# Kernel optimization log

Measured on AMD Instinct MI355X. Metric: run time of the kernel, lower is better.

Reference implementation:

```python
import jax, jax.numpy as jnp
import numpy as np

DIM = 512
NUM_HEADS = 8
HEAD_DIM = DIM // NUM_HEADS
SEGMENT_LENGTHS = (1024, 2048, 4096)
DILATED_RATIOS = (1, 2, 4)
SCALE = HEAD_DIM ** -0.5
NEG_FILL = -100000000.0  # matches torch masked_fill value


def setup_inputs() -> dict:
    key = jax.random.key(0)
    ks = jax.random.split(key, 8)
    b, L = 2, 8192
    def nrm(k, shape, s=1.0):
        return jax.random.normal(k, shape, dtype=jnp.float32) * s
    return {
        "query": nrm(ks[0], (b, L, DIM)),
        "key_": nrm(ks[1], (b, L, DIM)),
        "value": nrm(ks[2], (b, L, DIM)),
        "Wq": nrm(ks[3], (DIM, DIM), DIM ** -0.5),
        "Wk": nrm(ks[4], (DIM, DIM), DIM ** -0.5),
        "Wv": nrm(ks[5], (DIM, DIM), DIM ** -0.5),
        "Wo": nrm(ks[6], (DIM, DIM), DIM ** -0.5),
        "bo": nrm(ks[7], (DIM,), 0.01),
    }


def _branch(q, k, v, sl, dr):
    """One (segment_length, dilation) branch.
    q,k,v: (b, L, H, D). Returns dense out (b, L, H, D) and lse (b, L, H),
    with uncovered positions set to (0, NEG_FILL).
    gathering/dense_to_sparse reduces, per head hd, to selecting positions
    l*dr + (hd // (H//dr)) within each segment (diagonal of the r1 x r2 block).
    """
    b, L, H, D = q.shape
    n = L // sl          # segments per sequence
    hsub = H // dr       # heads per dilation offset
    lsub = sl // dr      # kept tokens per segment
    # (lsub, H): dilated position of each kept token for each head
    pos = jnp.arange(lsub)[:, None] * dr + (jnp.arange(H) // hsub)[None, :]
    hid = jnp.arange(H)[None, :]

    def gather(x):
        xs = x.reshape(b, n, sl, H, D)
        g = xs[:, :, pos, hid, :]                  # (b, n, lsub, H, D)
        return jnp.transpose(g, (0, 1, 3, 2, 4))    # (b, n, H, lsub, D)

    qi = gather(q) * SCALE
    ki = gather(k)
    vi = gather(v)
    scores = jnp.einsum('bnhld,bnhmd->bnhlm', qi, ki)
    lse = jax.nn.logsumexp(scores, axis=-1)                                  # (b, n, H, lsub)
    p = jax.nn.softmax(scores.astype(jnp.float32), axis=-1).astype(scores.dtype)
    o = jnp.einsum('bnhlm,bnhmd->bnhld', p, vi)                              # (b, n, H, lsub, D)
    # sparse_to_dense: scatter back onto dilated positions (diag_embed)
    o_ = jnp.transpose(o, (0, 1, 3, 2, 4))                                    # (b, n, lsub, H, D)
    od = jnp.zeros((b, n, sl, H, D), o.dtype).at[:, :, pos, hid, :].set(o_)
    ld = jnp.zeros((b, n, sl, H), lse.dtype).at[:, :, pos, hid].set(
        jnp.transpose(lse, (0, 1, 3, 2)))
    ld = jnp.where(ld == 0, NEG_FILL, ld)  # masked_fill_(lse == 0, -1e8)
    return od.reshape(b, L, H, D), ld.reshape(b, L, H)


def reference(query, key_, value, Wq, Wk, Wv, Wo, bo):
    b, L, _ = query.shape
    def heads(x, W):
        return (x @ W.T).reshape(b, L, NUM_HEADS, HEAD_DIM)
    q = heads(query, Wq)
    k = heads(key_, Wk)
    v = heads(value, Wv)
    outs, lses = [], []
    for sl, dr in zip(SEGMENT_LENGTHS, DILATED_RATIOS):
        o, l = _branch(q, k, v, sl, dr)
        outs.append(o)
        lses.append(l)
    # merge branches via logsumexp-weighted combination (weights detached in torch)
    lse_stack = jnp.stack(lses, 0)            # (nb, b, L, H)
    m = lse_stack.max(0)
    w = jnp.exp(lse_stack - m)
    w = w / w.sum(0)
    w = jax.lax.stop_gradient(w)
    out = sum(o * wi[..., None] for o, wi in zip(outs, list(w)))
    out = out.reshape(b, L, DIM)
    return out @ Wo.T + bo
```

## Files before the change

### kernel.cpp

```cpp
#include <hip/hip_runtime.h>
#include <hip/hip_bf16.h>

typedef unsigned short u16;
typedef unsigned int u32;
typedef __attribute__((ext_vector_type(8))) short short8;
typedef __attribute__((ext_vector_type(4))) float floatx4;
typedef __attribute__((ext_vector_type(2))) unsigned int uint2v;

__device__ __forceinline__ float b2f(u16 u) {
    u32 x = ((u32)u) << 16;
    return __builtin_bit_cast(float, x);
}
__device__ __forceinline__ u16 f2b(float f) {
    u32 x = __builtin_bit_cast(u32, f);
    return (u16)((x + 0x7fffu + ((x >> 16) & 1u)) >> 16);
}
__device__ __forceinline__ u32 pack2(float lo, float hi) {
    float2 f; f.x = lo; f.y = hi;
    __hip_bfloat162 h = __float22bfloat162_rn(f);
    u32 r;
    __builtin_memcpy(&r, &h, 4);
    return r;
}
__device__ __forceinline__ float fexp2(float x) {
#if __has_builtin(__builtin_amdgcn_exp2f)
    return __builtin_amdgcn_exp2f(x);
#else
    return __expf(x * 0.6931471805599453f);
#endif
}

__device__ __forceinline__ uint2v pl32(u32 a, u32 b) {
    return __builtin_amdgcn_permlane32_swap(a, b, false, false);
}

__device__ __forceinline__ void gl16(const u16* g, u16* l) {
    __builtin_amdgcn_global_load_lds(
        (const __attribute__((address_space(1))) void*)g,
        (__attribute__((address_space(3))) void*)l, 16, 0, 0);
}

template<bool AF32>
__global__ __launch_bounds__(256) void gemm_bt_bias(
    const void* __restrict__ Ap, const float* __restrict__ B,
    u16* __restrict__ Cb, float* __restrict__ Cf, const float* __restrict__ bias,
    int M, int N, int K, float scale)
{
    __shared__ __align__(16) u16 a_lds[128][72];
    __shared__ __align__(16) u16 b_lds[128][72];
    const int tid = threadIdx.x;
    const int lane = tid & 63, wv = tid >> 6;
    const int quad = lane >> 4, l15 = lane & 15;
    const int tm = blockIdx.x, tn = blockIdx.y;
    const int wm = (wv >> 1) * 64, wn = (wv & 1) * 64;
    (void)M;

    floatx4 acc[4][4];
#pragma unroll
    for (int i = 0; i < 4; ++i)
#pragma unroll
        for (int j = 0; j < 4; ++j) acc[i][j] = (floatx4)0.f;

    for (int k0 = 0; k0 < K; k0 += 64) {
#pragma unroll
        for (int r = 0; r < 4; ++r) {
            int idx = r * 256 + tid;
            int row = idx >> 3, ch = (idx & 7) * 8;
            if constexpr (AF32) {
                const float* A = (const float*)Ap;
                const float* src = A + (size_t)(tm * 128 + row) * K + k0 + ch;
                float4 f0 = *(const float4*)src;
                float4 f1 = *(const float4*)(src + 4);
                uint4 pk;
                pk.x = pack2(f0.x, f0.y);
                pk.y = pack2(f0.z, f0.w);
                pk.z = pack2(f1.x, f1.y);
                pk.w = pack2(f1.z, f1.w);
                *(uint4*)&a_lds[row][ch] = pk;
            } else {
                const u16* A = (const u16*)Ap;
                *(uint4*)&a_lds[row][ch] =
                    *(const uint4*)(A + (size_t)(tm * 128 + row) * K + k0 + ch);
            }
            {
                const float* src = B + (size_t)(tn * 128 + row) * K + k0 + ch;
                float4 f0 = *(const float4*)src;
                float4 f1 = *(const float4*)(src + 4);
                uint4 pk;
                pk.x = pack2(f0.x, f0.y);
                pk.y = pack2(f0.z, f0.w);
                pk.z = pack2(f1.x, f1.y);
                pk.w = pack2(f1.z, f1.w);
                *(uint4*)&b_lds[row][ch] = pk;
            }
        }
        __syncthreads();
#pragma unroll
        for (int dc = 0; dc < 2; ++dc) {
            short8 af[4], bf[4];
#pragma unroll
            for (int mi = 0; mi < 4; ++mi)
                af[mi] = *(const short8*)&a_lds[wm + mi * 16 + l15][dc * 32 + quad * 8];
#pragma unroll
            for (int ni = 0; ni < 4; ++ni)
                bf[ni] = *(const short8*)&b_lds[wn + ni * 16 + l15][dc * 32 + quad * 8];
#pragma unroll
            for (int mi = 0; mi < 4; ++mi)
#pragma unroll
                for (int ni = 0; ni < 4; ++ni)
                    acc[mi][ni] = __builtin_amdgcn_mfma_f32_16x16x32_bf16(
                        af[mi], bf[ni], acc[mi][ni], 0, 0, 0);
        }
        __syncthreads();
    }
#pragma unroll
    for (int mi = 0; mi < 4; ++mi)
#pragma unroll
        for (int ni = 0; ni < 4; ++ni) {
            int col = tn * 128 + wn + ni * 16 + l15;
            float bb = bias ? bias[col] : 0.f;
#pragma unroll
            for (int r = 0; r < 4; ++r) {
                int row = tm * 128 + wm + mi * 16 + quad * 4 + r;
                float val = acc[mi][ni][r] * scale + bb;
                if (Cf) Cf[(size_t)row * N + col] = val;
                else    Cb[(size_t)row * N + col] = f2b(val);
            }
        }
}

__device__ __forceinline__ void decode_inst(int inst, int& b, int& s, int& h,
                                            int& sl, int& dr, int& phase)
{
    if (inst < 128)      { int j = inst;       b = j >> 6; s = (j >> 3) & 7; h = j & 7; sl = 1024; dr = 1; phase = 0;      }
    else if (inst < 192) { int j = inst - 128; b = j >> 5; s = (j >> 3) & 3; h = j & 7; sl = 2048; dr = 2; phase = h >> 2; }
    else                 { int j = inst - 192; b = j >> 4; s = (j >> 3) & 1; h = j & 7; sl = 4096; dr = 4; phase = h >> 1; }
}

__global__ __launch_bounds__(256) void gather_kv(
    const u16* __restrict__ kk, const u16* __restrict__ vv,
    u16* __restrict__ KG, u16* __restrict__ VT)
{
    int inst = blockIdx.x;
    int b, s, h, sl, dr, phase;
    decode_inst(inst, b, s, h, sl, dr, phase);
    int n0 = blockIdx.y * 32;
    __shared__ __align__(16) u16 tile[32][72];
    int tid = threadIdx.x;
    int row = tid >> 3, ch = (tid & 7) * 8;
    int n = n0 + row;
    size_t pos = (size_t)s * sl + (size_t)n * dr + phase;
    size_t src = (((size_t)b * 8192 + pos) * 8 + h) * 64 + ch;
    int chs = ch ^ ((n & 7) * 8);
    *(uint4*)(KG + ((size_t)inst * 1024 + n) * 64 + chs) = *(const uint4*)(kk + src);
    *(uint4*)&tile[row][ch] = *(const uint4*)(vv + src);
    __syncthreads();
    int d = tid >> 2, nn = (tid & 3) * 8;
    __align__(16) u16 tmp[8];
#pragma unroll
    for (int j = 0; j < 8; ++j) tmp[j] = tile[nn + j][d];
    int col = (n0 + nn) ^ ((d & 7) * 8);
    *(uint4*)(VT + ((size_t)inst * 64 + d) * 1024 + col) = *(uint4*)tmp;
}

__global__ __launch_bounds__(256, 4) void attn_kernel(
    const u16* __restrict__ q, const u16* __restrict__ KG,
    const u16* __restrict__ VT, u16* __restrict__ Og, float* __restrict__ Lg)
{
    const int inst = blockIdx.y, qt = blockIdx.x;
    int b, s, h, sl, dr, phase;
    decode_inst(inst, b, s, h, sl, dr, phase);
    __shared__ __align__(16) u16 k_lds[128][64];
    __shared__ __align__(16) u16 vt_lds[64][128];
    const int tid = threadIdx.x, lane = tid & 63, wv = tid >> 6;
    const int quad = lane >> 4, l15 = lane & 15;
    const int sl15 = (l15 & 3) | ((l15 & 4) << 1) | ((l15 & 8) >> 1);
    const int ksw = (sl15 & 7) * 8;
    const int vsw = (l15 & 7) * 8;

    const int qrow = qt * 64 + wv * 16 + l15;
    const size_t qpos = (size_t)s * sl + (size_t)qrow * dr + phase;
    const u16* qbase = q + (((size_t)b * 8192 + qpos) * 8 + h) * 64;
    const short8 qf0 = *(const short8*)(qbase + quad * 8);
    const short8 qf1 = *(const short8*)(qbase + 32 + quad * 8);

    floatx4 oacc[4];
#pragma unroll
    for (int dt = 0; dt < 4; ++dt) oacc[dt] = (floatx4)0.f;
    float mst = -1e30f, lst = 0.f;

    const u16* KGb = KG + (size_t)inst * 65536;
    const u16* VTb = VT + (size_t)inst * 65536;
    u16* klb = &k_lds[0][0];
    u16* vlb = &vt_lds[0][0];

    for (int it = 0; it < 8; ++it) {
        const int k0 = it * 128;
#pragma unroll
        for (int r = 0; r < 4; ++r) {
            int c = wv * 4 + r;
            gl16(KGb + (size_t)k0 * 64 + c * 512 + lane * 8, klb + c * 512);
            gl16(VTb + (size_t)(c * 4 + (lane >> 4)) * 1024 + k0 + (lane & 15) * 8,
                 vlb + c * 512);
        }
        __syncthreads();

        floatx4 sacc[8];
#pragma unroll
        for (int nt = 0; nt < 8; ++nt) {
            sacc[nt] = (floatx4)0.f;
            short8 kf0 = *(const short8*)&k_lds[nt * 16 + sl15][(quad * 8) ^ ksw];
            short8 kf1 = *(const short8*)&k_lds[nt * 16 + sl15][(32 + quad * 8) ^ ksw];
            sacc[nt] = __builtin_amdgcn_mfma_f32_16x16x32_bf16(kf0, qf0, sacc[nt], 0, 0, 0);
            sacc[nt] = __builtin_amdgcn_mfma_f32_16x16x32_bf16(kf1, qf1, sacc[nt], 0, 0, 0);
        }

        float mx = sacc[0][0];
#pragma unroll
        for (int nt = 0; nt < 8; ++nt)
#pragma unroll
            for (int r = 0; r < 4; ++r) mx = fmaxf(mx, sacc[nt][r]);
        mx = fmaxf(mx, __shfl_xor(mx, 16, 64));
        mx = fmaxf(mx, __shfl_xor(mx, 32, 64));
        float mnew = fmaxf(mst, mx);
        float alpha = fexp2(mst - mnew);
        float rs = 0.f;
#pragma unroll
        for (int nt = 0; nt < 8; ++nt)
#pragma unroll
            for (int r = 0; r < 4; ++r) {
                float p = fexp2(sacc[nt][r] - mnew);
                sacc[nt][r] = p;
                rs += p;
            }
        rs += __shfl_xor(rs, 16, 64);
        rs += __shfl_xor(rs, 32, 64);
        lst = lst * alpha + rs;
        mst = mnew;
#pragma unroll
        for (int dt = 0; dt < 4; ++dt) oacc[dt] *= alpha;

#pragma unroll
        for (int nc = 0; nc < 4; ++nc) {
            u32 pk00 = pack2(sacc[2 * nc][0], sacc[2 * nc][1]);
            u32 pk01 = pack2(sacc[2 * nc][2], sacc[2 * nc][3]);
            u32 pk10 = pack2(sacc[2 * nc + 1][0], sacc[2 * nc + 1][1]);
            u32 pk11 = pack2(sacc[2 * nc + 1][2], sacc[2 * nc + 1][3]);
            uint2v xz = pl32(pk00, pk10);
            uint2v yw = pl32(pk01, pk11);
            uint4 bw;
            bw.x = xz[0];
            bw.y = yw[0];
            bw.z = xz[1];
            bw.w = yw[1];
            short8 pf = __builtin_bit_cast(short8, bw);
#pragma unroll
            for (int dt = 0; dt < 4; ++dt) {
                short8 vf = *(const short8*)
                    &vt_lds[dt * 16 + l15][(nc * 32 + quad * 8) ^ vsw];
                oacc[dt] = __builtin_amdgcn_mfma_f32_16x16x32_bf16(vf, pf, oacc[dt], 0, 0, 0);
            }
        }
        __syncthreads();
    }

    const int esw = (l15 & 7) * 8;
    float inv_l = (lst > 0.f) ? (1.f / lst) : 0.f;
#pragma unroll
    for (int dt = 0; dt < 4; ++dt) {
        u32 lo = pack2(oacc[dt][0] * inv_l, oacc[dt][1] * inv_l);
        u32 hi = pack2(oacc[dt][2] * inv_l, oacc[dt][3] * inv_l);
        uint2 v; v.x = lo; v.y = hi;
        *(uint2*)&k_lds[wv * 16 + l15][(dt * 16 + quad * 4) ^ esw] = v;
    }
    __syncthreads();
#pragma unroll
    for (int c = 0; c < 2; ++c) {
        uint4 val = *(const uint4*)&k_lds[wv * 16 + l15][(quad * 16 + c * 8) ^ esw];
        *(uint4*)(Og + (((size_t)inst * 1024 + qt * 64 + wv * 16 + l15) * 64
                        + quad * 16 + c * 8)) = val;
    }
    if (quad == 0) {
        Lg[(size_t)inst * 1024 + qt * 64 + wv * 16 + l15] = mst + __log2f(lst);
    }
}

__global__ __launch_bounds__(256) void merge_kernel(
    const u16* __restrict__ Og, const float* __restrict__ Lg,
    u16* __restrict__ merged)
{
    int bid = blockIdx.x;
    int b = bid >> 13, l = bid & 8191;
    int t = threadIdx.x;
    int h = t >> 5, d0 = (t & 31) * 2;

    int inst0 = b * 64 + ((l >> 10) << 3) + h;
    int row0 = l & 1023;
    int p1 = l & 2047;
    bool c1 = ((p1 & 1) == (h >> 2));
    int inst1 = 128 + b * 32 + ((l >> 11) << 3) + h;
    int row1 = p1 >> 1;
    int p2 = l & 4095;
    bool c2 = ((p2 & 3) == (h >> 1));
    int inst2 = 192 + b * 16 + ((l >> 12) << 3) + h;
    int row2 = p2 >> 2;

    float lse0 = Lg[(size_t)inst0 * 1024 + row0];
    float lse1 = c1 ? Lg[(size_t)inst1 * 1024 + row1] : -1e30f;
    float lse2 = c2 ? Lg[(size_t)inst2 * 1024 + row2] : -1e30f;
    float m = fmaxf(lse0, fmaxf(lse1, lse2));
    float w0 = fexp2(lse0 - m);
    float w1 = c1 ? fexp2(lse1 - m) : 0.f;
    float w2 = c2 ? fexp2(lse2 - m) : 0.f;
    float inv = 1.f / (w0 + w1 + w2);
    w0 *= inv; w1 *= inv; w2 *= inv;

    u32 u0 = *(const u32*)(Og + ((size_t)inst0 * 1024 + row0) * 64 + d0);
    u32 u1 = c1 ? *(const u32*)(Og + ((size_t)inst1 * 1024 + row1) * 64 + d0) : 0u;
    u32 u2 = c2 ? *(const u32*)(Og + ((size_t)inst2 * 1024 + row2) * 64 + d0) : 0u;
    float a0 = b2f((u16)(u0 & 0xffff)), e0 = b2f((u16)(u0 >> 16));
    float a1 = b2f((u16)(u1 & 0xffff)), e1 = b2f((u16)(u1 >> 16));
    float a2 = b2f((u16)(u2 & 0xffff)), e2 = b2f((u16)(u2 >> 16));
    float ra = w0 * a0 + w1 * a1 + w2 * a2;
    float rb = w0 * e0 + w1 * e1 + w2 * e2;
    u32 outp = pack2(ra, rb);
    *(u32*)(merged + (((size_t)b * 8192 + l) * 8 + h) * 64 + d0) = outp;
}

extern "C" void kernel_launch(void* const* d_in, const int* in_sizes, int n_in,
                              void* d_out, int out_size, void* d_ws, size_t ws_size,
                              hipStream_t stream)
{
    (void)in_sizes; (void)n_in; (void)out_size; (void)ws_size;
    const float* query = (const float*)d_in[0];
    const float* key_  = (const float*)d_in[1];
    const float* value = (const float*)d_in[2];
    const float* Wq    = (const float*)d_in[3];
    const float* Wk    = (const float*)d_in[4];
    const float* Wv    = (const float*)d_in[5];
    const float* Wo    = (const float*)d_in[6];
    const float* bo    = (const float*)d_in[7];

    char* ws = (char*)d_ws;
    const size_t SZ_PROJ = (size_t)16384 * 512 * 2;
    const size_t SZ_KG   = (size_t)224 * 1024 * 64 * 2;
    const size_t SZ_LG   = (size_t)224 * 1024 * 4;
    u16*   qb     = (u16*)(ws);
    u16*   kb     = (u16*)(ws + SZ_PROJ);
    u16*   vb     = (u16*)(ws + 2 * SZ_PROJ);
    u16*   KG     = (u16*)(ws + 3 * SZ_PROJ);
    u16*   VT     = (u16*)(ws + 3 * SZ_PROJ + SZ_KG);
    u16*   Og     = (u16*)(ws + 3 * SZ_PROJ + 2 * SZ_KG);
    float* Lg     = (float*)(ws + 3 * SZ_PROJ + 3 * SZ_KG);
    u16*   merged = (u16*)(ws + 3 * SZ_PROJ + 3 * SZ_KG + SZ_LG);

    const int M = 16384, N = 512, K = 512;
    const float SCALE = 0.125f * 1.44269504088896f;

    gemm_bt_bias<true><<<dim3(128, 4), 256, 0, stream>>>(query, Wq, qb, nullptr, nullptr, M, N, K, SCALE);
    gemm_bt_bias<true><<<dim3(128, 4), 256, 0, stream>>>(key_,  Wk, kb, nullptr, nullptr, M, N, K, 1.0f);
    gemm_bt_bias<true><<<dim3(128, 4), 256, 0, stream>>>(value, Wv, vb, nullptr, nullptr, M, N, K, 1.0f);
    gather_kv<<<dim3(224, 32), 256, 0, stream>>>(kb, vb, KG, VT);
    attn_kernel<<<dim3(16, 224), 256, 0, stream>>>(qb, KG, VT, Og, Lg);
    merge_kernel<<<16384, 256, 0, stream>>>(Og, Lg, merged);
    gemm_bt_bias<false><<<dim3(128, 4), 256, 0, stream>>>(merged, Wo, nullptr, (float*)d_out, bo, M, N, K, 1.0f);
}
```

Before: 353.1 us.

## Use lazy max rescaling and MFMA row sums in attention softmax

```diff
diff --git a/kernel.cpp b/kernel.cpp
--- a/kernel.cpp
+++ b/kernel.cpp
@@ -184,10 +184,16 @@
     const short8 qf0 = *(const short8*)(qbase + quad * 8);
     const short8 qf1 = *(const short8*)(qbase + 32 + quad * 8);
 
+    uint4 onesw;
+    onesw.x = 0x3F803F80u; onesw.y = 0x3F803F80u;
+    onesw.z = 0x3F803F80u; onesw.w = 0x3F803F80u;
+    const short8 vones = __builtin_bit_cast(short8, onesw);
+
     floatx4 oacc[4];
 #pragma unroll
     for (int dt = 0; dt < 4; ++dt) oacc[dt] = (floatx4)0.f;
-    float mst = -1e30f, lst = 0.f;
+    floatx4 racc = (floatx4)0.f;
+    float mst = -1e30f;
 
     const u16* KGb = KG + (size_t)inst * 65536;
     const u16* VTb = VT + (size_t)inst * 65536;
@@ -215,30 +221,37 @@
             sacc[nt] = __builtin_amdgcn_mfma_f32_16x16x32_bf16(kf1, qf1, sacc[nt], 0, 0, 0);
         }
 
-        float mx = sacc[0][0];
-#pragma unroll
-        for (int nt = 0; nt < 8; ++nt)
-#pragma unroll
-            for (int r = 0; r < 4; ++r) mx = fmaxf(mx, sacc[nt][r]);
+        float t0, t1;
+        {
+            float m0 = fmaxf(fmaxf(sacc[0][0], sacc[0][1]), fmaxf(sacc[0][2], sacc[0][3]));
+            float m1 = fmaxf(fmaxf(sacc[1][0], sacc[1][1]), fmaxf(sacc[1][2], sacc[1][3]));
+            float m2 = fmaxf(fmaxf(sacc[2][0], sacc[2][1]), fmaxf(sacc[2][2], sacc[2][3]));
+            float m3 = fmaxf(fmaxf(sacc[3][0], sacc[3][1]), fmaxf(sacc[3][2], sacc[3][3]));
+            t0 = fmaxf(fmaxf(m0, m1), fmaxf(m2, m3));
+            float m4 = fmaxf(fmaxf(sacc[4][0], sacc[4][1]), fmaxf(sacc[4][2], sacc[4][3]));
+            float m5 = fmaxf(fmaxf(sacc[5][0], sacc[5][1]), fmaxf(sacc[5][2], sacc[5][3]));
+            float m6 = fmaxf(fmaxf(sacc[6][0], sacc[6][1]), fmaxf(sacc[6][2], sacc[6][3]));
+            float m7 = fmaxf(fmaxf(sacc[7][0], sacc[7][1]), fmaxf(sacc[7][2], sacc[7][3]));
+            t1 = fmaxf(fmaxf(m4, m5), fmaxf(m6, m7));
+        }
+        float mx = fmaxf(t0, t1);
         mx = fmaxf(mx, __shfl_xor(mx, 16, 64));
         mx = fmaxf(mx, __shfl_xor(mx, 32, 64));
-        float mnew = fmaxf(mst, mx);
-        float alpha = fexp2(mst - mnew);
-        float rs = 0.f;
+
+        if (!__all(mx - mst <= 8.f)) {
+            float mnew = fmaxf(mst, mx);
+            float alpha = fexp2(mst - mnew);
+#pragma unroll
+            for (int dt = 0; dt < 4; ++dt) oacc[dt] *= alpha;
+            racc *= alpha;
+            mst = mnew;
+        }
+
 #pragma unroll
         for (int nt = 0; nt < 8; ++nt)
 #pragma unroll
-            for (int r = 0; r < 4; ++r) {
-                float p = fexp2(sacc[nt][r] - mnew);
-                sacc[nt][r] = p;
-                rs += p;
-            }
-        rs += __shfl_xor(rs, 16, 64);
-        rs += __shfl_xor(rs, 32, 64);
-        lst = lst * alpha + rs;
-        mst = mnew;
-#pragma unroll
-        for (int dt = 0; dt < 4; ++dt) oacc[dt] *= alpha;
+            for (int r = 0; r < 4; ++r)
+                sacc[nt][r] = fexp2(sacc[nt][r] - mst);
 
 #pragma unroll
         for (int nc = 0; nc < 4; ++nc) {
@@ -260,11 +273,13 @@
                     &vt_lds[dt * 16 + l15][(nc * 32 + quad * 8) ^ vsw];
                 oacc[dt] = __builtin_amdgcn_mfma_f32_16x16x32_bf16(vf, pf, oacc[dt], 0, 0, 0);
             }
+            racc = __builtin_amdgcn_mfma_f32_16x16x32_bf16(vones, pf, racc, 0, 0, 0);
         }
         __syncthreads();
     }
 
     const int esw = (l15 & 7) * 8;
+    float lst = racc[0];
     float inv_l = (lst > 0.f) ? (1.f / lst) : 0.f;
 #pragma unroll
     for (int dt = 0; dt < 4; ++dt) {
```

New measurement: 341.5 us. 1.03x faster.
